# Kernel tuning notes

Hardware: AMD Instinct MI355X
Metric: run time of the kernel (lower is better)

## Reference

```python
import jax, jax.numpy as jnp
import numpy as np

D_MODEL = 1024
N_HEADS = 16


def setup_inputs() -> dict:
    key = jax.random.key(0)
    ks = jax.random.split(key, 16)
    B, L, S, D = 4, 2048, 2048, D_MODEL
    inp = {
        "q": jax.random.normal(ks[0], (B, L, D), jnp.float32),
        "k": jax.random.normal(ks[1], (B, S, D), jnp.float32),
        "v": jax.random.normal(ks[2], (B, S, D), jnp.float32),
        "tau": jax.random.uniform(ks[3], (B, 1), jnp.float32, 0.5, 1.5),
        "delta": jax.random.normal(ks[4], (B, S), jnp.float32),
    }
    s = 1.0 / np.sqrt(D)
    inp["Wq"] = jax.random.normal(ks[5], (D, D), jnp.float32) * s
    inp["bq"] = jnp.zeros((D,), jnp.float32)
    inp["Wk"] = jax.random.normal(ks[6], (D, D), jnp.float32) * s
    inp["bk"] = jnp.zeros((D,), jnp.float32)
    inp["Wv"] = jax.random.normal(ks[7], (D, D), jnp.float32) * s
    inp["bv"] = jnp.zeros((D,), jnp.float32)
    inp["Wo"] = jax.random.normal(ks[8], (D, D), jnp.float32) * s
    inp["bo"] = jnp.zeros((D,), jnp.float32)
    return inp


def reference(q, k, v, tau, delta, Wq, bq, Wk, bk, Wv, bv, Wo, bo):
    B, L, D = q.shape
    S = k.shape[1]
    H = N_HEADS
    E = D // H
    # Linear projections (torch Linear: x @ W.T + b), split heads
    qh = (q @ Wq.T + bq).reshape(B, L, H, E)
    kh = (k @ Wk.T + bk).reshape(B, S, H, E)
    vh = (v @ Wv.T + bv).reshape(B, S, H, E)
    scale = 1.0 / np.sqrt(E).astype(np.float32)
    # de-stationary attention: scores * tau + delta, then scaled softmax
    scores = jnp.einsum('blhe,bshe->bhls', qh, kh)
    scores = scores * tau[:, None, None, :] + delta[:, None, None, :]
    a = jax.nn.softmax(scale * scores, axis=-1)  # dropout: eval mode (identity)
    out = jnp.einsum('bhls,bshd->blhd', a, vh).reshape(B, L, D)
    return out @ Wo.T + bo
```

## Files before the change

kernel.cpp:

```cpp
#include <hip/hip_runtime.h>
#include <hip/hip_bf16.h>
#include <stdint.h>

typedef unsigned short u16;
typedef __attribute__((ext_vector_type(8))) short short8;
typedef __attribute__((ext_vector_type(4))) short short4v;
typedef __attribute__((ext_vector_type(4))) float f32x4;
typedef __attribute__((ext_vector_type(16))) float f32x16;
typedef __attribute__((ext_vector_type(2))) unsigned int uint2v;
typedef __attribute__((ext_vector_type(4))) unsigned int uint4v;

#define DEV static __device__ __forceinline__

DEV u16 f2bf(float f) {
  union { float f; unsigned u; } x; x.f = f;
  unsigned r = x.u + 0x7FFFu + ((x.u >> 16) & 1u);
  return (u16)(r >> 16);
}

DEV unsigned cvtpk_bf16(float a, float b) {
  unsigned r;
  asm("v_cvt_pk_bf16_f32 %0, %1, %2" : "=v"(r) : "v"(a), "v"(b));
  return r;
}

DEV void pl32swap(unsigned& a, unsigned& b) {
  asm("v_permlane32_swap_b32 %0, %1" : "+v"(a), "+v"(b));
}

DEV void gld_lds16(const void* g, void* l) {
  __builtin_amdgcn_global_load_lds(
      (const __attribute__((address_space(1))) unsigned int*)(g),
      (__attribute__((address_space(3))) unsigned int*)(l),
      16, 0, 0);
}

DEV f32x16 zero16() {
  f32x16 z = {0.f,0.f,0.f,0.f,0.f,0.f,0.f,0.f,0.f,0.f,0.f,0.f,0.f,0.f,0.f,0.f};
  return z;
}

__global__ void cvt3(const float* __restrict__ a, const float* __restrict__ b,
                     const float* __restrict__ c, u16* __restrict__ oa,
                     u16* __restrict__ ob, u16* __restrict__ oc, int n4) {
  int i = blockIdx.x * blockDim.x + threadIdx.x;
  if (i >= n4) return;
  const float* in = (blockIdx.y == 0) ? a : (blockIdx.y == 1) ? b : c;
  u16* out = (blockIdx.y == 0) ? oa : (blockIdx.y == 1) ? ob : oc;
  float4 v = ((const float4*)in)[i];
  short4v o;
  o[0] = (short)f2bf(v.x); o[1] = (short)f2bf(v.y);
  o[2] = (short)f2bf(v.z); o[3] = (short)f2bf(v.w);
  ((short4v*)out)[i] = o;
}

__global__ void cvt4(const float* __restrict__ a, const float* __restrict__ b,
                     const float* __restrict__ c, const float* __restrict__ d,
                     u16* __restrict__ oa, u16* __restrict__ ob,
                     u16* __restrict__ oc, u16* __restrict__ od, int n4) {
  int i = blockIdx.x * blockDim.x + threadIdx.x;
  if (i >= n4) return;
  const float* in = (blockIdx.y == 0) ? a : (blockIdx.y == 1) ? b : (blockIdx.y == 2) ? c : d;
  u16* out = (blockIdx.y == 0) ? oa : (blockIdx.y == 1) ? ob : (blockIdx.y == 2) ? oc : od;
  float4 v = ((const float4*)in)[i];
  short4v o;
  o[0] = (short)f2bf(v.x); o[1] = (short)f2bf(v.y);
  o[2] = (short)f2bf(v.z); o[3] = (short)f2bf(v.w);
  ((short4v*)out)[i] = o;
}

__global__ void scale_delta(const float* __restrict__ in, float* __restrict__ out, int n4) {
  int i = blockIdx.x * blockDim.x + threadIdx.x;
  if (i >= n4) return;
  constexpr float C = 0.125f * 1.44269504f;
  float4 v = ((const float4*)in)[i];
  f32x4 o = {v.x * C, v.y * C, v.z * C, v.w * C};
  ((f32x4*)out)[i] = o;
}

__global__ __launch_bounds__(256, 2)
void gemm_qkv(const u16* __restrict__ A, const u16* __restrict__ W,
              const float* __restrict__ bq, const float* __restrict__ bk,
              const float* __restrict__ bv, u16* __restrict__ qhb,
              u16* __restrict__ khb, u16* __restrict__ vtb) {
  constexpr int Nn = 1024, Kn = 1024;
  constexpr int BM = 128, BN = 128, BK = 64;
  __shared__ __align__(16) u16 As[BM * BK];
  __shared__ __align__(16) u16 Bs[BN * BK];
  constexpr int nbn = Nn / BN;
  constexpr int nwg = (24576 / BM) * nbn;
  int bid = blockIdx.x;
  int swz = (bid & 7) * (nwg >> 3) + (bid >> 3);
  int bm = (swz / nbn) * BM;
  int bn = (swz % nbn) * BN;
  int mat = bm >> 13;
  int bml = bm & 8191;
  int tid = threadIdx.x;
  int lane = tid & 63, w = tid >> 6;
  int l15 = lane & 15, l4 = lane >> 4;
  int wm = (w >> 1) * 64, wn = (w & 1) * 64;
  int swl = (w << 6);

  f32x4 acc[4][4];
#pragma unroll
  for (int i = 0; i < 4; ++i)
#pragma unroll
    for (int j = 0; j < 4; ++j) acc[i][j] = (f32x4){0.f, 0.f, 0.f, 0.f};

  const u16* Ag = A + (size_t)bm * Kn;
  const u16* Bg = W + ((size_t)mat << 20) + (size_t)bn * Kn;

  for (int kt = 0; kt < Kn / BK; ++kt) {
    int k0 = kt * BK;
#pragma unroll
    for (int j = 0; j < 4; ++j) {
      int flat = j * 256 + tid;
      int row = flat >> 3, u = flat & 7;
      int gu = u ^ (row & 7);
      gld_lds16(Ag + (size_t)row * Kn + k0 + gu * 8, &As[(j * 256 + swl) * 8]);
    }
#pragma unroll
    for (int j = 0; j < 4; ++j) {
      int flat = j * 256 + tid;
      int row = flat >> 3, u = flat & 7;
      int gu = u ^ (row & 7);
      gld_lds16(Bg + (size_t)row * Kn + k0 + gu * 8, &Bs[(j * 256 + swl) * 8]);
    }
    __syncthreads();
#pragma unroll
    for (int ks = 0; ks < 2; ++ks) {
      short8 af[4], bfr[4];
#pragma unroll
      for (int i = 0; i < 4; ++i) {
        int ra = wm + i * 16 + l15;
        int ua = (ks * 4 + l4) ^ (ra & 7);
        af[i] = *(const short8*)&As[ra * 64 + ua * 8];
        int rb = wn + i * 16 + l15;
        int ub = (ks * 4 + l4) ^ (rb & 7);
        bfr[i] = *(const short8*)&Bs[rb * 64 + ub * 8];
      }
#pragma unroll
      for (int mi = 0; mi < 4; ++mi)
#pragma unroll
        for (int ni = 0; ni < 4; ++ni)
          acc[mi][ni] = __builtin_amdgcn_mfma_f32_16x16x32_bf16(af[mi], bfr[ni], acc[mi][ni], 0, 0, 0);
    }
    __syncthreads();
  }

  const float* bias = (mat == 0) ? bq : (mat == 1) ? bk : bv;
  u16* oQK = (mat == 0) ? qhb : khb;
#pragma unroll
  for (int ni = 0; ni < 4; ++ni) {
    int n = bn + wn + ni * 16 + l15;
    float bvl = bias[n];
    int h = n >> 6, e = n & 63;
#pragma unroll
    for (int mi = 0; mi < 4; ++mi) {
      int m0 = bml + wm + mi * 16 + l4 * 4;
      if (mat < 2) {
#pragma unroll
        for (int j = 0; j < 4; ++j) {
          int m = m0 + j;
          int b = m >> 11, l = m & 2047;
          int idx = ((b * 16 + h) * 2048 + l) * 64 + e;
          oQK[idx] = f2bf(acc[mi][ni][j] + bvl);
        }
      } else {
        int b = m0 >> 11, s = m0 & 2047;
        short4v pk;
#pragma unroll
        for (int j = 0; j < 4; ++j) pk[j] = (short)f2bf(acc[mi][ni][j] + bvl);
        int idx = ((b * 16 + h) * 64 + e) * 2048 + s;
        *(short4v*)&vtb[idx] = pk;
      }
    }
  }
}

__global__ __launch_bounds__(256, 2)
void gemm_out(const u16* __restrict__ A, const u16* __restrict__ Bt,
              const float* __restrict__ bias, float* __restrict__ out) {
  constexpr int Nn = 1024, Kn = 1024;
  constexpr int BM = 128, BN = 128, BK = 64;
  __shared__ __align__(16) u16 As[BM * BK];
  __shared__ __align__(16) u16 Bs[BN * BK];
  constexpr int nbn = Nn / BN;
  constexpr int nwg = (8192 / BM) * nbn;
  int bid = blockIdx.x;
  int swz = (bid & 7) * (nwg >> 3) + (bid >> 3);
  int bm = (swz / nbn) * BM;
  int bn = (swz % nbn) * BN;
  int tid = threadIdx.x;
  int lane = tid & 63, w = tid >> 6;
  int l15 = lane & 15, l4 = lane >> 4;
  int wm = (w >> 1) * 64, wn = (w & 1) * 64;
  int swl = (w << 6);

  f32x4 acc[4][4];
#pragma unroll
  for (int i = 0; i < 4; ++i)
#pragma unroll
    for (int j = 0; j < 4; ++j) acc[i][j] = (f32x4){0.f, 0.f, 0.f, 0.f};

  const u16* Ag = A + (size_t)bm * Kn;
  const u16* Bg = Bt + (size_t)bn * Kn;

  for (int kt = 0; kt < Kn / BK; ++kt) {
    int k0 = kt * BK;
#pragma unroll
    for (int j = 0; j < 4; ++j) {
      int flat = j * 256 + tid;
      int row = flat >> 3, u = flat & 7;
      int gu = u ^ (row & 7);
      gld_lds16(Ag + (size_t)row * Kn + k0 + gu * 8, &As[(j * 256 + swl) * 8]);
    }
#pragma unroll
    for (int j = 0; j < 4; ++j) {
      int flat = j * 256 + tid;
      int row = flat >> 3, u = flat & 7;
      int gu = u ^ (row & 7);
      gld_lds16(Bg + (size_t)row * Kn + k0 + gu * 8, &Bs[(j * 256 + swl) * 8]);
    }
    __syncthreads();
#pragma unroll
    for (int ks = 0; ks < 2; ++ks) {
      short8 af[4], bfr[4];
#pragma unroll
      for (int i = 0; i < 4; ++i) {
        int ra = wm + i * 16 + l15;
        int ua = (ks * 4 + l4) ^ (ra & 7);
        af[i] = *(const short8*)&As[ra * 64 + ua * 8];
        int rb = wn + i * 16 + l15;
        int ub = (ks * 4 + l4) ^ (rb & 7);
        bfr[i] = *(const short8*)&Bs[rb * 64 + ub * 8];
      }
#pragma unroll
      for (int mi = 0; mi < 4; ++mi)
#pragma unroll
        for (int ni = 0; ni < 4; ++ni)
          acc[mi][ni] = __builtin_amdgcn_mfma_f32_16x16x32_bf16(af[mi], bfr[ni], acc[mi][ni], 0, 0, 0);
    }
    __syncthreads();
  }

#pragma unroll
  for (int ni = 0; ni < 4; ++ni) {
    int n = bn + wn + ni * 16 + l15;
    float bvl = bias[n];
#pragma unroll
    for (int mi = 0; mi < 4; ++mi) {
      int m0 = bm + wm + mi * 16 + l4 * 4;
#pragma unroll
      for (int j = 0; j < 4; ++j)
        out[(size_t)(m0 + j) * Nn + n] = acc[mi][ni][j] + bvl;
    }
  }
}

DEV float softpack(const f32x16 sc, float st2, const float* dlp, int hi,
                   short8& f0, short8& f1) {
  float pe[16];
#pragma unroll
  for (int g = 0; g < 4; ++g) {
    f32x4 dlv = *(const f32x4*)(dlp + g * 8 + hi * 4);
#pragma unroll
    for (int m = 0; m < 4; ++m)
      pe[g * 4 + m] = __builtin_amdgcn_exp2f(sc[g * 4 + m] * st2 + dlv[m]);
  }
  float ps = 0.f;
#pragma unroll
  for (int i = 0; i < 16; i += 4) ps += (pe[i] + pe[i + 1]) + (pe[i + 2] + pe[i + 3]);
  unsigned a0 = cvtpk_bf16(pe[0], pe[1]), a1 = cvtpk_bf16(pe[2], pe[3]);
  unsigned b0 = cvtpk_bf16(pe[4], pe[5]), b1 = cvtpk_bf16(pe[6], pe[7]);
  pl32swap(a0, b0);
  pl32swap(a1, b1);
  f0 = __builtin_bit_cast(short8, (uint4v){a0, a1, b0, b1});
  unsigned c0 = cvtpk_bf16(pe[8], pe[9]), c1 = cvtpk_bf16(pe[10], pe[11]);
  unsigned d0 = cvtpk_bf16(pe[12], pe[13]), d1 = cvtpk_bf16(pe[14], pe[15]);
  pl32swap(c0, d0);
  pl32swap(c1, d1);
  f1 = __builtin_bit_cast(short8, (uint4v){c0, c1, d0, d1});
  return ps;
}

__global__ __launch_bounds__(256, 4)
void flash_attn(const u16* __restrict__ qh, const u16* __restrict__ kh,
                const u16* __restrict__ vt, const float* __restrict__ tau,
                const float* __restrict__ dl2g, u16* __restrict__ attn) {
  constexpr int S = 2048, E = 64;
  __shared__ __align__(16) u16 Ks[2][4096];
  __shared__ __align__(16) u16 Vs[2][4096];
  __shared__ __align__(16) float dls[2][64];

  int bh = blockIdx.x & 63, qb = blockIdx.x >> 6;
  int b = bh >> 4, h = bh & 15;
  int tid = threadIdx.x, lane = tid & 63, w = tid >> 6;
  int l31 = lane & 31, hi = lane >> 5;
  int q0 = qb * 128 + w * 32;

  const u16* Kg = kh + (size_t)bh * S * E;
  const u16* Vg = vt + (size_t)bh * E * S;
  const float* Dg = dl2g + (size_t)b * S;

  const u16* Qg = qh + ((size_t)bh * S + q0) * E;
  short8 qf[4];
#pragma unroll
  for (int ec = 0; ec < 4; ++ec)
    qf[ec] = *(const short8*)&Qg[l31 * E + ec * 16 + hi * 8];

  float st2 = tau[b] * (0.125f * 1.44269504f);
  float l_run = 0.f;
  f32x16 oa0 = zero16(), oa1 = zero16();

#pragma unroll
  for (int r = 0; r < 2; ++r) {
    int c = r * 4 + w;
    gld_lds16(Kg + (size_t)lane * E + c * 8, &Ks[0][(r * 256 + w * 64) * 8]);
    gld_lds16(Vg + (size_t)lane * S + c * 8, &Vs[0][(r * 256 + w * 64) * 8]);
  }
  if (tid < 16) gld_lds16(Dg + tid * 4, &dls[0][0]);
  __syncthreads();

  int kvbase = hi * 1024 + l31 * 16;

  for (int t = 0; t < S / 64; ++t) {
    int cur = t & 1, nxt = cur ^ 1;
    if (t < S / 64 - 1) {
      int s1 = (t + 1) * 64;
#pragma unroll
      for (int r = 0; r < 2; ++r) {
        int c = r * 4 + w;
        gld_lds16(Kg + (size_t)(s1 + lane) * E + c * 8, &Ks[nxt][(r * 256 + w * 64) * 8]);
        gld_lds16(Vg + (size_t)lane * S + s1 + c * 8, &Vs[nxt][(r * 256 + w * 64) * 8]);
      }
      if (tid < 16) gld_lds16(Dg + s1 + tid * 4, &dls[nxt][0]);
    }

    const char* KsB = (const char*)&Ks[cur][0];
    f32x16 sc0 = zero16(), sc1 = zero16();
    __builtin_amdgcn_s_setprio(1);
#pragma unroll
    for (int ec = 0; ec < 4; ++ec) {
      short8 kf0 = *(const short8*)(KsB + kvbase + ec * 2048);
      short8 kf1 = *(const short8*)(KsB + kvbase + ec * 2048 + 512);
      sc0 = __builtin_amdgcn_mfma_f32_32x32x16_bf16(kf0, qf[ec], sc0, 0, 0, 0);
      sc1 = __builtin_amdgcn_mfma_f32_32x32x16_bf16(kf1, qf[ec], sc1, 0, 0, 0);
    }
    __builtin_amdgcn_s_setprio(0);

    short8 pf0, pf1, pf2, pf3;
    float psum = softpack(sc0, st2, &dls[cur][0], hi, pf0, pf1);
    psum += softpack(sc1, st2, &dls[cur][32], hi, pf2, pf3);
    psum += __shfl_xor(psum, 32);
    l_run += psum;

    const char* VsB = (const char*)&Vs[cur][0];
    __builtin_amdgcn_s_setprio(1);
#pragma unroll
    for (int ksb = 0; ksb < 4; ++ksb) {
      short8 v0 = *(const short8*)(VsB + kvbase + ksb * 2048);
      short8 v1 = *(const short8*)(VsB + kvbase + ksb * 2048 + 512);
      short8 pf = (ksb == 0) ? pf0 : (ksb == 1) ? pf1 : (ksb == 2) ? pf2 : pf3;
      oa0 = __builtin_amdgcn_mfma_f32_32x32x16_bf16(v0, pf, oa0, 0, 0, 0);
      oa1 = __builtin_amdgcn_mfma_f32_32x32x16_bf16(v1, pf, oa1, 0, 0, 0);
    }
    __builtin_amdgcn_s_setprio(0);
    __syncthreads();
  }

  float li = 1.f / l_run;
  u16* Og = attn + ((((size_t)b * 2048 + q0 + l31) * 16 + h) * 64);
#pragma unroll
  for (int g = 0; g < 4; ++g) {
    uint2v s0, s1;
    s0[0] = cvtpk_bf16(oa0[g * 4 + 0] * li, oa0[g * 4 + 1] * li);
    s0[1] = cvtpk_bf16(oa0[g * 4 + 2] * li, oa0[g * 4 + 3] * li);
    *(uint2v*)&Og[g * 8 + hi * 4] = s0;
    s1[0] = cvtpk_bf16(oa1[g * 4 + 0] * li, oa1[g * 4 + 1] * li);
    s1[1] = cvtpk_bf16(oa1[g * 4 + 2] * li, oa1[g * 4 + 3] * li);
    *(uint2v*)&Og[32 + g * 8 + hi * 4] = s1;
  }
}

extern "C" void kernel_launch(void* const* d_in, const int* in_sizes, int n_in,
                              void* d_out, int out_size, void* d_ws, size_t ws_size,
                              hipStream_t stream) {
  const float* q = (const float*)d_in[0];
  const float* k = (const float*)d_in[1];
  const float* v = (const float*)d_in[2];
  const float* tau = (const float*)d_in[3];
  const float* delta = (const float*)d_in[4];
  const float* Wq = (const float*)d_in[5];
  const float* bq = (const float*)d_in[6];
  const float* Wk = (const float*)d_in[7];
  const float* bk = (const float*)d_in[8];
  const float* Wv = (const float*)d_in[9];
  const float* bv = (const float*)d_in[10];
  const float* Wo = (const float*)d_in[11];
  const float* bo = (const float*)d_in[12];

  const size_t SZ_ACT = (size_t)8192 * 1024 * 2;
  const size_t SZ_W = (size_t)1024 * 1024 * 2;
  char* p = (char*)d_ws;
  u16* qbf = (u16*)p; p += SZ_ACT;
  u16* kbf = (u16*)p; p += SZ_ACT;
  u16* vbf = (u16*)p; p += SZ_ACT;
  u16* wq = (u16*)p; p += SZ_W;
  u16* wk = (u16*)p; p += SZ_W;
  u16* wv = (u16*)p; p += SZ_W;
  u16* wo = (u16*)p; p += SZ_W;
  float* dl2g = (float*)p; p += 8192 * 4;
  u16* qhb = (u16*)p; p += SZ_ACT;
  u16* khb = (u16*)p; p += SZ_ACT;
  u16* vtb = (u16*)p; p += SZ_ACT;
  u16* attn = qbf;

  cvt3<<<dim3(8192, 3), 256, 0, stream>>>(q, k, v, qbf, kbf, vbf, 2097152);
  cvt4<<<dim3(1024, 4), 256, 0, stream>>>(Wq, Wk, Wv, Wo, wq, wk, wv, wo, 262144);
  scale_delta<<<8, 256, 0, stream>>>(delta, dl2g, 2048);

  gemm_qkv<<<1536, 256, 0, stream>>>(qbf, wq, bq, bk, bv, qhb, khb, vtb);
  flash_attn<<<1024, 256, 0, stream>>>(qhb, khb, vtb, tau, dl2g, attn);
  gemm_out<<<512, 256, 0, stream>>>(attn, wo, bo, (float*)d_out);
}
```

Baseline: 220.7 us.

## Stage K/V through registers into XOR-swizzled LDS to avoid bank conflicts

Replaces the direct global-to-LDS loads for K and V tiles with register-staged global loads that are written into LDS after the compute phase, using an XOR-swizzled layout. The MFMA fragment reads use matching swizzled offsets so they no longer hit the same LDS banks. The goal is to remove LDS bank conflicts on the fragment reads and to hide global load latency behind the current tile's MFMAs. In exchange it uses more VGPRs for the in-flight tiles and adds explicit LDS store instructions.

```diff
diff --git a/kernel.cpp b/kernel.cpp
--- a/kernel.cpp
+++ b/kernel.cpp
@@ -303,6 +303,12 @@
   const u16* Vg = vt + (size_t)bh * E * S;
   const float* Dg = dl2g + (size_t)b * S;
 
+  int wbyte = (tid & 7) * 1024 + ((tid >> 3) ^ (tid & 7)) * 16;
+  int rb0 = (hi) * 1024 + ((l31 ^ (hi)) * 16);
+  int rb1 = (2 + hi) * 1024 + ((l31 ^ (2 + hi)) * 16);
+  int rb2 = (4 + hi) * 1024 + ((l31 ^ (4 + hi)) * 16);
+  int rb3 = (6 + hi) * 1024 + ((l31 ^ (6 + hi)) * 16);
+
   const u16* Qg = qh + ((size_t)bh * S + q0) * E;
   short8 qf[4];
 #pragma unroll
@@ -313,39 +319,57 @@
   float l_run = 0.f;
   f32x16 oa0 = zero16(), oa1 = zero16();
 
-#pragma unroll
-  for (int r = 0; r < 2; ++r) {
-    int c = r * 4 + w;
-    gld_lds16(Kg + (size_t)lane * E + c * 8, &Ks[0][(r * 256 + w * 64) * 8]);
-    gld_lds16(Vg + (size_t)lane * S + c * 8, &Vs[0][(r * 256 + w * 64) * 8]);
+  short8 k0, k1, v0, v1;
+  {
+    k0 = *(const short8*)(Kg + (size_t)tid * 8);
+    k1 = *(const short8*)(Kg + (size_t)(256 + tid) * 8);
+    v0 = *(const short8*)(Vg + (size_t)(tid >> 3) * S + (tid & 7) * 8);
+    v1 = *(const short8*)(Vg + (size_t)(32 + (tid >> 3)) * S + (tid & 7) * 8);
   }
   if (tid < 16) gld_lds16(Dg + tid * 4, &dls[0][0]);
+  {
+    char* KsB = (char*)&Ks[0][0];
+    char* VsB = (char*)&Vs[0][0];
+    *(short8*)(KsB + wbyte) = k0;
+    *(short8*)(KsB + wbyte + 512) = k1;
+    *(short8*)(VsB + wbyte) = v0;
+    *(short8*)(VsB + wbyte + 512) = v1;
+  }
   __syncthreads();
 
-  int kvbase = hi * 1024 + l31 * 16;
-
-  for (int t = 0; t < S / 64; ++t) {
-    int cur = t & 1, nxt = cur ^ 1;
-    if (t < S / 64 - 1) {
+#pragma unroll 2
+  for (int t = 0; t < 32; ++t) {
+    int cur = t & 1;
+    bool pf = (t < 31);
+    if (pf) {
       int s1 = (t + 1) * 64;
-#pragma unroll
-      for (int r = 0; r < 2; ++r) {
-        int c = r * 4 + w;
-        gld_lds16(Kg + (size_t)(s1 + lane) * E + c * 8, &Ks[nxt][(r * 256 + w * 64) * 8]);
-        gld_lds16(Vg + (size_t)lane * S + s1 + c * 8, &Vs[nxt][(r * 256 + w * 64) * 8]);
-      }
-      if (tid < 16) gld_lds16(Dg + s1 + tid * 4, &dls[nxt][0]);
+      k0 = *(const short8*)(Kg + (size_t)s1 * 64 + (size_t)tid * 8);
+      k1 = *(const short8*)(Kg + (size_t)s1 * 64 + (size_t)(256 + tid) * 8);
+      v0 = *(const short8*)(Vg + (size_t)(tid >> 3) * S + s1 + (tid & 7) * 8);
+      v1 = *(const short8*)(Vg + (size_t)(32 + (tid >> 3)) * S + s1 + (tid & 7) * 8);
+      if (tid < 16) gld_lds16(Dg + s1 + tid * 4, &dls[cur ^ 1][0]);
     }
 
     const char* KsB = (const char*)&Ks[cur][0];
     f32x16 sc0 = zero16(), sc1 = zero16();
     __builtin_amdgcn_s_setprio(1);
-#pragma unroll
-    for (int ec = 0; ec < 4; ++ec) {
-      short8 kf0 = *(const short8*)(KsB + kvbase + ec * 2048);
-      short8 kf1 = *(const short8*)(KsB + kvbase + ec * 2048 + 512);
-      sc0 = __builtin_amdgcn_mfma_f32_32x32x16_bf16(kf0, qf[ec], sc0, 0, 0, 0);
-      sc1 = __builtin_amdgcn_mfma_f32_32x32x16_bf16(kf1, qf[ec], sc1, 0, 0, 0);
+    {
+      short8 a0 = *(const short8*)(KsB + rb0);
+      short8 a1 = *(const short8*)(KsB + rb0 + 512);
+      sc0 = __builtin_amdgcn_mfma_f32_32x32x16_bf16(a0, qf[0], sc0, 0, 0, 0);
+      sc1 = __builtin_amdgcn_mfma_f32_32x32x16_bf16(a1, qf[0], sc1, 0, 0, 0);
+      a0 = *(const short8*)(KsB + rb1);
+      a1 = *(const short8*)(KsB + rb1 + 512);
+      sc0 = __builtin_amdgcn_mfma_f32_32x32x16_bf16(a0, qf[1], sc0, 0, 0, 0);
+      sc1 = __builtin_amdgcn_mfma_f32_32x32x16_bf16(a1, qf[1], sc1, 0, 0, 0);
+      a0 = *(const short8*)(KsB + rb2);
+      a1 = *(const short8*)(KsB + rb2 + 512);
+      sc0 = __builtin_amdgcn_mfma_f32_32x32x16_bf16(a0, qf[2], sc0, 0, 0, 0);
+      sc1 = __builtin_amdgcn_mfma_f32_32x32x16_bf16(a1, qf[2], sc1, 0, 0, 0);
+      a0 = *(const short8*)(KsB + rb3);
+      a1 = *(const short8*)(KsB + rb3 + 512);
+      sc0 = __builtin_amdgcn_mfma_f32_32x32x16_bf16(a0, qf[3], sc0, 0, 0, 0);
+      sc1 = __builtin_amdgcn_mfma_f32_32x32x16_bf16(a1, qf[3], sc1, 0, 0, 0);
     }
     __builtin_amdgcn_s_setprio(0);
 
@@ -357,15 +381,34 @@
 
     const char* VsB = (const char*)&Vs[cur][0];
     __builtin_amdgcn_s_setprio(1);
-#pragma unroll
-    for (int ksb = 0; ksb < 4; ++ksb) {
-      short8 v0 = *(const short8*)(VsB + kvbase + ksb * 2048);
-      short8 v1 = *(const short8*)(VsB + kvbase + ksb * 2048 + 512);
-      short8 pf = (ksb == 0) ? pf0 : (ksb == 1) ? pf1 : (ksb == 2) ? pf2 : pf3;
-      oa0 = __builtin_amdgcn_mfma_f32_32x32x16_bf16(v0, pf, oa0, 0, 0, 0);
-      oa1 = __builtin_amdgcn_mfma_f32_32x32x16_bf16(v1, pf, oa1, 0, 0, 0);
+    {
+      short8 a0 = *(const short8*)(VsB + rb0);
+      short8 a1 = *(const short8*)(VsB + rb0 + 512);
+      oa0 = __builtin_amdgcn_mfma_f32_32x32x16_bf16(a0, pf0, oa0, 0, 0, 0);
+      oa1 = __builtin_amdgcn_mfma_f32_32x32x16_bf16(a1, pf0, oa1, 0, 0, 0);
+      a0 = *(const short8*)(VsB + rb1);
+      a1 = *(const short8*)(VsB + rb1 + 512);
+      oa0 = __builtin_amdgcn_mfma_f32_32x32x16_bf16(a0, pf1, oa0, 0, 0, 0);
+      oa1 = __builtin_amdgcn_mfma_f32_32x32x16_bf16(a1, pf1, oa1, 0, 0, 0);
+      a0 = *(const short8*)(VsB + rb2);
+      a1 = *(const short8*)(VsB + rb2 + 512);
+      oa0 = __builtin_amdgcn_mfma_f32_32x32x16_bf16(a0, pf2, oa0, 0, 0, 0);
+      oa1 = __builtin_amdgcn_mfma_f32_32x32x16_bf16(a1, pf2, oa1, 0, 0, 0);
+      a0 = *(const short8*)(VsB + rb3);
+      a1 = *(const short8*)(VsB + rb3 + 512);
+      oa0 = __builtin_amdgcn_mfma_f32_32x32x16_bf16(a0, pf3, oa0, 0, 0, 0);
+      oa1 = __builtin_amdgcn_mfma_f32_32x32x16_bf16(a1, pf3, oa1, 0, 0, 0);
     }
     __builtin_amdgcn_s_setprio(0);
+
+    if (pf) {
+      char* KsW = (char*)&Ks[cur ^ 1][0];
+      char* VsW = (char*)&Vs[cur ^ 1][0];
+      *(short8*)(KsW + wbyte) = k0;
+      *(short8*)(KsW + wbyte + 512) = k1;
+      *(short8*)(VsW + wbyte) = v0;
+      *(short8*)(VsW + wbyte + 512) = v1;
+    }
     __syncthreads();
   }
 
```

Measured after the change: 207.1 us. 1.07x faster.
